# Optimization experiments

Hardware: AMD Instinct MI355X
Metric: run time of the kernel (lower is better)

## Reference

```python
import jax, jax.numpy as jnp
import numpy as np

N_NODES = 50000
N_EDGES = 800000
C_IN = 64
C_OUT = 64
K = 3


def setup_inputs() -> dict:
    key = jax.random.key(0)
    k1, k2, k3, k4, k5, k6 = jax.random.split(key, 6)
    x = jax.random.normal(k1, (N_NODES, C_IN), dtype=jnp.float32)
    edge_index = jax.random.randint(k2, (2, N_EDGES), 0, N_NODES, dtype=jnp.int32)
    edge_weight = jax.random.uniform(k3, (N_EDGES,), dtype=jnp.float32)
    # Xavier-uniform init for [K, C_IN, C_OUT] (fan over last two dims)
    limit = float(np.sqrt(6.0 / (C_IN + C_OUT)))
    theta_forward = jax.random.uniform(k4, (K, C_IN, C_OUT), minval=-limit, maxval=limit, dtype=jnp.float32)
    theta_backward = jax.random.uniform(k5, (K, C_IN, C_OUT), minval=-limit, maxval=limit, dtype=jnp.float32)
    return {
        "x": x,
        "edge_index": edge_index,
        "edge_weight": edge_weight,
        "theta_forward": theta_forward,
        "theta_backward": theta_backward,
    }


def _propagate(x, row, col, edge_weight, n_nodes):
    # degree normalization: deg[i] = sum of edge_weight over edges with row == i
    deg = jax.ops.segment_sum(edge_weight, row, num_segments=n_nodes)
    deg_inv = jnp.where(deg > 0, jax.lax.rsqrt(jnp.where(deg > 0, deg, 1.0)), 0.0)
    norm = deg_inv[row] * edge_weight * deg_inv[col]      # [E]
    msg = norm[:, None] * x[col]                          # [E, C] gather-scale
    return jax.ops.segment_sum(msg, row, num_segments=n_nodes)  # scatter-add -> [N, C]


def reference(x, edge_index, edge_weight, theta_forward, theta_backward):
    row, col = edge_index[0], edge_index[1]
    n_nodes = x.shape[0]
    k = theta_forward.shape[0]
    Tx_0 = x
    Tx_1 = _propagate(x, row, col, edge_weight, n_nodes)
    out = Tx_0 @ theta_forward[0] + Tx_1 @ theta_backward[0]
    for i in range(1, k):
        Tx_2 = _propagate(Tx_1, row, col, edge_weight, n_nodes)
        out = out + Tx_2 @ theta_forward[i] + Tx_1 @ theta_backward[i]
        Tx_1 = Tx_2
    return out
```

## Files before the change

### kernel.cpp

```cpp
#include <hip/hip_runtime.h>
#include <hip/hip_fp16.h>


#define N_NODES 50000
#define N_EDGES 800000
#define C 64
#define CAP 64
#define NPART 196
#define CAPP 4608
#define EPB 8192
#define NEB 98
#define XH_BLOCKS 782
#define CW_BLOCKS 16
#define NPADL 50176
#define NSLICE 4
#define PB 3125
#define GB 782

typedef _Float16 half8 __attribute__((ext_vector_type(8)));
typedef float f32x4 __attribute__((ext_vector_type(4)));

__global__ __launch_bounds__(1024) void scatter2_kernel(
        const int* __restrict__ row, const int* __restrict__ col,
        const float* __restrict__ w, int* __restrict__ percur,
        uint2* __restrict__ pedges,
        const float* __restrict__ x, __half* __restrict__ xh,
        const float* __restrict__ tf, const float* __restrict__ tb,
        _Float16* __restrict__ whc) {
    const int tid = threadIdx.x;
    if (blockIdx.x >= NEB + XH_BLOCKS) {
        int idx = (blockIdx.x - NEB - XH_BLOCKS) * 1024 + tid;
        int j = idx >> 12;
        int rem = idx & 4095;
        int ci = rem >> 6;
        int co = rem & 63;
        float v;
        if (j == 0)      v = tf[rem];
        else if (j == 1) v = tb[rem] + tb[4096 + rem];
        else if (j == 2) v = tf[4096 + rem] + tb[8192 + rem];
        else             v = tf[8192 + rem];
        whc[(j << 12) + (co << 6) + ci] = (_Float16)v;
        return;
    }
    if (blockIdx.x >= NEB) {
        int i = (blockIdx.x - NEB) * 1024 + tid;
        if (i < N_NODES * C / 4) {
            float4 v = ((const float4*)x)[i];
            union { float2 f2; __half2 h2[2]; } u;
            u.h2[0] = __floats2half2_rn(v.x, v.y);
            u.h2[1] = __floats2half2_rn(v.z, v.w);
            int node = i >> 4;
            int ci0 = (i & 15) << 2;
            int slice = ci0 >> 4;
            int off = ci0 & 15;
            *(float2*)(void*)(xh + (((size_t)slice * NPADL + node) << 4) + off)
                = u.f2;
        }
        return;
    }
    __shared__ int h[NPART];
    __shared__ int cur[NPART];
    uint2 ent[8];
    int pp[8];
    if (tid < NPART) h[tid] = 0;
    __syncthreads();
    int base = blockIdx.x * EPB;
#pragma unroll
    for (int i = 0; i < 8; ++i) {
        int e = base + i * 1024 + tid;
        pp[i] = -1;
        if (e < N_EDGES) {
            int r = row[e];
            unsigned int c = (unsigned int)col[e];
            unsigned int wh = (unsigned int)__half_as_ushort(__float2half_rn(w[e]));
            ent[i] = make_uint2((c << 16) | wh, (unsigned int)(r & 255));
            pp[i] = r >> 8;
            atomicAdd(&h[pp[i]], 1);
        }
    }
    __syncthreads();
    if (tid < NPART) cur[tid] = atomicAdd(&percur[tid], h[tid]);
    __syncthreads();
#pragma unroll
    for (int i = 0; i < 8; ++i) {
        if (pp[i] >= 0) {
            int slot = atomicAdd(&cur[pp[i]], 1);
            pedges[(size_t)pp[i] * CAPP + slot] = ent[i];
        }
    }
}

__global__ __launch_bounds__(1024) void build_kernel(
        const uint2* __restrict__ pedges, const int* __restrict__ percur,
        unsigned int* __restrict__ bkt, int* __restrict__ cnt,
        float* __restrict__ dinv) {
    __shared__ unsigned int lbuck[256 * CAP];
    __shared__ int lcnt[256];
    const int tid = threadIdx.x;
    const int p = blockIdx.x;
    if (tid < 256) lcnt[tid] = 0;
    __syncthreads();
    int e = min(percur[p], CAPP);
    const uint2* src = pedges + (size_t)p * CAPP;
    for (int i = tid; i < e; i += 1024) {
        uint2 en = src[i];
        int rl = (int)en.y;
        int slot = atomicAdd(&lcnt[rl], 1);
        if (slot < CAP) lbuck[(rl << 6) + slot] = en.x;
    }
    __syncthreads();
    if (tid < 256) {
        int m = min(lcnt[tid], CAP);
        int g = (p << 8) + tid;
        float sum = 0.f;
        for (int j = 0; j < m; ++j)
            sum += __half2float(__ushort_as_half(
                (unsigned short)(lbuck[(tid << 6) + j] & 0xFFFFu)));
        if (g < N_NODES) {
            cnt[g] = m;
            dinv[g] = (sum > 0.f) ? rsqrtf(sum) : 0.f;
        }
    }
    __syncthreads();
    {
        int r = tid >> 2;
        int ch = tid & 3;
        int m = min(lcnt[r], CAP);
        const uint4* s4 = (const uint4*)&lbuck[r << 6];
        uint4* dst = (uint4*)(bkt + (((size_t)(p << 8) + r) << 6));
        for (int j = ch; (j << 2) < m; j += 4) dst[j] = s4[j];
    }
}

__global__ __launch_bounds__(1024) void decode_kernel(
        const unsigned int* __restrict__ bkt, const int* __restrict__ cnt,
        const float* __restrict__ dinv, unsigned int* __restrict__ bkt2) {
    int e = blockIdx.x * 1024 + threadIdx.x;
    int node = e >> 6;
    int j = e & 63;
    if (node < N_NODES && j < min(cnt[node], CAP)) {
        unsigned int b = bkt[e];
        int c = (int)(b >> 16);
        float nn = __half2float(__ushort_as_half((unsigned short)(b & 0xFFFFu)))
                   * dinv[c];
        bkt2[e] = ((unsigned int)c << 16) |
                  (unsigned int)__half_as_ushort(__float2half_rn(nn));
    }
}

__global__ __launch_bounds__(256) void prop_kernel(
        const __half* __restrict__ xin, __half* __restrict__ xout,
        const int* __restrict__ cnt, const unsigned int* __restrict__ bkt2,
        const float* __restrict__ dinv) {
    const int tid = threadIdx.x;
    const int wib = tid >> 6;
    const int lane = tid & 63;
    const int q = lane >> 4;
    const int ql = lane & 15;
    const int u = ql >> 2;
    const int cq = ql & 3;
    const int slice = blockIdx.x & 3;
    const int tile = blockIdx.x >> 2;
    const int node = (tile << 4) + (wib << 2) + q;
    const int m = min(cnt[node], CAP);
    const int base = node << 6;
    int cj[4];
    float nj[4];
#pragma unroll
    for (int s = 0; s < 4; ++s) {
        int idx = (s << 4) + ql;
        cj[s] = 0;
        nj[s] = 0.f;
        if (idx < m) {
            unsigned int b = bkt2[base + idx];
            cj[s] = (int)(b >> 16) << 4;
            nj[s] = __half2float(__ushort_as_half((unsigned short)(b & 0xFFFFu)));
        }
    }
    int mx = m;
    mx = max(mx, __shfl_xor(mx, 16));
    mx = max(mx, __shfl_xor(mx, 32));
    const __half* xsl = xin + ((size_t)slice * NPADL << 4);
    float a0 = 0.f, a1 = 0.f, a2 = 0.f, a3 = 0.f;
    {
        int cs[8];
        float ns[8];
        float2 vs[8];
#pragma unroll
        for (int g = 0; g < 2; ++g)
#pragma unroll
            for (int t = 0; t < 4; ++t) {
                int i = (g << 2) + t;
                int sl = (q << 4) + (t << 2) + u;
                cs[i] = __shfl(cj[g], sl);
                ns[i] = __shfl(nj[g], sl);
            }
#pragma unroll
        for (int i = 0; i < 8; ++i)
            vs[i] = *(const float2*)(xsl + cs[i] + (cq << 2));
#pragma unroll
        for (int i = 0; i < 8; ++i) {
            const __half2* hp = (const __half2*)&vs[i];
            float2 A = __half22float2(hp[0]);
            float2 B = __half22float2(hp[1]);
            a0 += ns[i] * A.x;
            a1 += ns[i] * A.y;
            a2 += ns[i] * B.x;
            a3 += ns[i] * B.y;
        }
    }
    if (mx > 32) {
        int cs[8];
        float ns[8];
        float2 vs[8];
#pragma unroll
        for (int g = 0; g < 2; ++g)
#pragma unroll
            for (int t = 0; t < 4; ++t) {
                int i = (g << 2) + t;
                int sl = (q << 4) + (t << 2) + u;
                cs[i] = __shfl(cj[2 + g], sl);
                ns[i] = __shfl(nj[2 + g], sl);
            }
#pragma unroll
        for (int i = 0; i < 8; ++i)
            vs[i] = *(const float2*)(xsl + cs[i] + (cq << 2));
#pragma unroll
        for (int i = 0; i < 8; ++i) {
            const __half2* hp = (const __half2*)&vs[i];
            float2 A = __half22float2(hp[0]);
            float2 B = __half22float2(hp[1]);
            a0 += ns[i] * A.x;
            a1 += ns[i] * A.y;
            a2 += ns[i] * B.x;
            a3 += ns[i] * B.y;
        }
    }
    a0 += __shfl_xor(a0, 4); a0 += __shfl_xor(a0, 8);
    a1 += __shfl_xor(a1, 4); a1 += __shfl_xor(a1, 8);
    a2 += __shfl_xor(a2, 4); a2 += __shfl_xor(a2, 8);
    a3 += __shfl_xor(a3, 4); a3 += __shfl_xor(a3, 8);
    if (u == 0) {
        float dr = dinv[node];
        union { float2 f2; __half2 h2[2]; } o;
        o.h2[0] = __floats2half2_rn(dr * a0, dr * a1);
        o.h2[1] = __floats2half2_rn(dr * a2, dr * a3);
        *(float2*)(void*)(xout + (((size_t)slice * NPADL + node) << 4)
                          + (cq << 2)) = o.f2;
    }
}

__global__ __launch_bounds__(256) void gemm_mfma_kernel(
        const __half* __restrict__ x0, const __half* __restrict__ x1,
        const __half* __restrict__ x2, const __half* __restrict__ x3,
        const _Float16* __restrict__ whc, float* __restrict__ out) {
    const int tid = threadIdx.x;
    const int wv = tid >> 6;
    const int lane = tid & 63;
    const int quad = lane >> 4;
    const int l16 = lane & 15;
    const int mbase = (blockIdx.x << 6) + (wv << 4);
    const __half* srcs[4] = {x0, x1, x2, x3};
    f32x4 acc0 = {}, acc1 = {}, acc2 = {}, acc3 = {};
    const int arow = mbase + l16;
    const bool aok = arow < N_NODES;
    const half8 zero8 = {};
#pragma unroll
    for (int j = 0; j < 4; ++j) {
        const __half* src = srcs[j];
#pragma unroll
        for (int kk = 0; kk < 64; kk += 32) {
            const int k0 = kk + (quad << 3);
            const int slice = k0 >> 4;
            const int koff = k0 & 15;
            half8 af = aok ? *(const half8*)(const void*)(
                src + (((size_t)slice * NPADL + arow) << 4) + koff) : zero8;
            const _Float16* wb = whc + (j << 12) + kk + (quad << 3);
            half8 b0 = *(const half8*)(const void*)(wb + ((0 * 16 + l16) << 6));
            half8 b1 = *(const half8*)(const void*)(wb + ((1 * 16 + l16) << 6));
            half8 b2 = *(const half8*)(const void*)(wb + ((2 * 16 + l16) << 6));
            half8 b3 = *(const half8*)(const void*)(wb + ((3 * 16 + l16) << 6));
            acc0 = __builtin_amdgcn_mfma_f32_16x16x32_f16(af, b0, acc0, 0, 0, 0);
            acc1 = __builtin_amdgcn_mfma_f32_16x16x32_f16(af, b1, acc1, 0, 0, 0);
            acc2 = __builtin_amdgcn_mfma_f32_16x16x32_f16(af, b2, acc2, 0, 0, 0);
            acc3 = __builtin_amdgcn_mfma_f32_16x16x32_f16(af, b3, acc3, 0, 0, 0);
        }
    }
#pragma unroll
    for (int i = 0; i < 4; ++i) {
        int r = mbase + (quad << 2) + i;
        if (r < N_NODES) {
            float* dst = out + ((size_t)r << 6) + l16;
            dst[0]  = acc0[i];
            dst[16] = acc1[i];
            dst[32] = acc2[i];
            dst[48] = acc3[i];
        }
    }
}

extern "C" void kernel_launch(void* const* d_in, const int* in_sizes, int n_in,
                              void* d_out, int out_size, void* d_ws, size_t ws_size,
                              hipStream_t stream) {
    const float* x  = (const float*)d_in[0];
    const int*   ei = (const int*)d_in[1];
    const float* ew = (const float*)d_in[2];
    const float* tf = (const float*)d_in[3];
    const float* tb = (const float*)d_in[4];
    float* out = (float*)d_out;

    const int* row = ei;
    const int* col = ei + N_EDGES;

    const size_t TBL = (size_t)NSLICE * NPADL * 16 / 2;
    float* ws = (float*)d_ws;
    size_t off = 0;
    int*    percur = (int*)(ws + off); off += 256;
    uint2*  pedges = (uint2*)(ws + off); off += (size_t)NPART * CAPP * 2;
    unsigned int* bkt  = (unsigned int*)(ws + off); off += (size_t)NPADL * CAP;
    unsigned int* bkt2 = (unsigned int*)(ws + off); off += (size_t)NPADL * CAP;
    int*    cnt  = (int*)(ws + off); off += NPADL;
    float*  dinv = ws + off; off += NPADL;
    __half* xh   = (__half*)(ws + off); off += TBL;
    __half* tA   = (__half*)(ws + off); off += TBL;
    __half* tB   = (__half*)(ws + off); off += TBL;
    __half* tC   = (__half*)(ws + off); off += TBL;
    _Float16* whc = (_Float16*)(ws + off); off += 4 * 64 * 64 / 2;

    hipMemsetAsync(percur, 0, 256 * sizeof(int), stream);

    scatter2_kernel<<<NEB + XH_BLOCKS + CW_BLOCKS, 1024, 0, stream>>>(
        row, col, ew, percur, pedges, x, xh, tf, tb, whc);
    build_kernel<<<NPART, 1024, 0, stream>>>(pedges, percur, bkt, cnt, dinv);
    decode_kernel<<<NPADL * CAP / 1024, 1024, 0, stream>>>(bkt, cnt, dinv, bkt2);

    prop_kernel<<<NSLICE * PB, 256, 0, stream>>>(xh, tA, cnt, bkt2, dinv);
    prop_kernel<<<NSLICE * PB, 256, 0, stream>>>(tA, tB, cnt, bkt2, dinv);
    prop_kernel<<<NSLICE * PB, 256, 0, stream>>>(tB, tC, cnt, bkt2, dinv);

    gemm_mfma_kernel<<<GB, 256, 0, stream>>>(xh, tA, tB, tC, whc, out);
}
```

Measured before the change: 185.4 us.

## Compact per-node edge buckets into CSR layout via two-level prefix scan

Replaces the fixed 64-slot-per-node bucket layout read by the propagation kernels with a compact CSR layout. Offsets come from a per-partition block scan in build_kernel plus a new single-block scan over partition totals. Each node's edges become contiguous with its neighbours' edges, so the three prop passes read fewer, denser cache lines of edge data. The cost is an extra tiny kernel launch, extra scan barriers in build, and two more index loads per node in prop.

```diff
diff --git a/kernel.cpp b/kernel.cpp
--- a/kernel.cpp
+++ b/kernel.cpp
@@ -93,9 +93,11 @@
 __global__ __launch_bounds__(1024) void build_kernel(
         const uint2* __restrict__ pedges, const int* __restrict__ percur,
         unsigned int* __restrict__ bkt, int* __restrict__ cnt,
-        float* __restrict__ dinv) {
+        float* __restrict__ dinv, int* __restrict__ loc,
+        int* __restrict__ tot) {
     __shared__ unsigned int lbuck[256 * CAP];
     __shared__ int lcnt[256];
+    __shared__ int sscan[256];
     const int tid = threadIdx.x;
     const int p = blockIdx.x;
     if (tid < 256) lcnt[tid] = 0;
@@ -120,6 +122,21 @@
             cnt[g] = m;
             dinv[g] = (sum > 0.f) ? rsqrtf(sum) : 0.f;
         }
+        sscan[tid] = m;
+    }
+    __syncthreads();
+#pragma unroll
+    for (int d = 1; d < 256; d <<= 1) {
+        int t = 0;
+        if (tid < 256 && tid >= d) t = sscan[tid - d];
+        __syncthreads();
+        if (tid < 256) sscan[tid] += t;
+        __syncthreads();
+    }
+    if (tid < 256) {
+        int m = min(lcnt[tid], CAP);
+        loc[(p << 8) + tid] = sscan[tid] - m;
+        if (tid == 255) tot[p] = sscan[255];
     }
     __syncthreads();
     {
@@ -132,9 +149,27 @@
     }
 }
 
+__global__ __launch_bounds__(256) void scan2_kernel(
+        const int* __restrict__ tot, int* __restrict__ btot) {
+    __shared__ int s[256];
+    const int tid = threadIdx.x;
+    int v = (tid < NPART) ? tot[tid] : 0;
+    s[tid] = v;
+    __syncthreads();
+#pragma unroll
+    for (int d = 1; d < 256; d <<= 1) {
+        int t = (tid >= d) ? s[tid - d] : 0;
+        __syncthreads();
+        s[tid] += t;
+        __syncthreads();
+    }
+    if (tid < NPART) btot[tid] = s[tid] - v;
+}
+
 __global__ __launch_bounds__(1024) void decode_kernel(
         const unsigned int* __restrict__ bkt, const int* __restrict__ cnt,
-        const float* __restrict__ dinv, unsigned int* __restrict__ bkt2) {
+        const float* __restrict__ dinv, const int* __restrict__ loc,
+        const int* __restrict__ btot, unsigned int* __restrict__ bkt2) {
     int e = blockIdx.x * 1024 + threadIdx.x;
     int node = e >> 6;
     int j = e & 63;
@@ -143,7 +178,7 @@
         int c = (int)(b >> 16);
         float nn = __half2float(__ushort_as_half((unsigned short)(b & 0xFFFFu)))
                    * dinv[c];
-        bkt2[e] = ((unsigned int)c << 16) |
+        bkt2[btot[node >> 8] + loc[node] + j] = ((unsigned int)c << 16) |
                   (unsigned int)__half_as_ushort(__float2half_rn(nn));
     }
 }
@@ -151,7 +186,8 @@
 __global__ __launch_bounds__(256) void prop_kernel(
         const __half* __restrict__ xin, __half* __restrict__ xout,
         const int* __restrict__ cnt, const unsigned int* __restrict__ bkt2,
-        const float* __restrict__ dinv) {
+        const float* __restrict__ dinv, const int* __restrict__ loc,
+        const int* __restrict__ btot) {
     const int tid = threadIdx.x;
     const int wib = tid >> 6;
     const int lane = tid & 63;
@@ -163,7 +199,7 @@
     const int tile = blockIdx.x >> 2;
     const int node = (tile << 4) + (wib << 2) + q;
     const int m = min(cnt[node], CAP);
-    const int base = node << 6;
+    const int csr = btot[node >> 8] + loc[node];
     int cj[4];
     float nj[4];
 #pragma unroll
@@ -172,7 +208,7 @@
         cj[s] = 0;
         nj[s] = 0.f;
         if (idx < m) {
-            unsigned int b = bkt2[base + idx];
+            unsigned int b = bkt2[csr + idx];
             cj[s] = (int)(b >> 16) << 4;
             nj[s] = __half2float(__ushort_as_half((unsigned short)(b & 0xFFFFu)));
         }
@@ -316,10 +352,13 @@
     float* ws = (float*)d_ws;
     size_t off = 0;
     int*    percur = (int*)(ws + off); off += 256;
+    int*    tot    = (int*)(ws + off); off += 256;
+    int*    btot   = (int*)(ws + off); off += 256;
     uint2*  pedges = (uint2*)(ws + off); off += (size_t)NPART * CAPP * 2;
     unsigned int* bkt  = (unsigned int*)(ws + off); off += (size_t)NPADL * CAP;
     unsigned int* bkt2 = (unsigned int*)(ws + off); off += (size_t)NPADL * CAP;
     int*    cnt  = (int*)(ws + off); off += NPADL;
+    int*    loc  = (int*)(ws + off); off += NPADL;
     float*  dinv = ws + off; off += NPADL;
     __half* xh   = (__half*)(ws + off); off += TBL;
     __half* tA   = (__half*)(ws + off); off += TBL;
@@ -331,12 +370,18 @@
 
     scatter2_kernel<<<NEB + XH_BLOCKS + CW_BLOCKS, 1024, 0, stream>>>(
         row, col, ew, percur, pedges, x, xh, tf, tb, whc);
-    build_kernel<<<NPART, 1024, 0, stream>>>(pedges, percur, bkt, cnt, dinv);
-    decode_kernel<<<NPADL * CAP / 1024, 1024, 0, stream>>>(bkt, cnt, dinv, bkt2);
-
-    prop_kernel<<<NSLICE * PB, 256, 0, stream>>>(xh, tA, cnt, bkt2, dinv);
-    prop_kernel<<<NSLICE * PB, 256, 0, stream>>>(tA, tB, cnt, bkt2, dinv);
-    prop_kernel<<<NSLICE * PB, 256, 0, stream>>>(tB, tC, cnt, bkt2, dinv);
+    build_kernel<<<NPART, 1024, 0, stream>>>(pedges, percur, bkt, cnt, dinv,
+                                             loc, tot);
+    scan2_kernel<<<1, 256, 0, stream>>>(tot, btot);
+    decode_kernel<<<NPADL * CAP / 1024, 1024, 0, stream>>>(
+        bkt, cnt, dinv, loc, btot, bkt2);
+
+    prop_kernel<<<NSLICE * PB, 256, 0, stream>>>(
+        xh, tA, cnt, bkt2, dinv, loc, btot);
+    prop_kernel<<<NSLICE * PB, 256, 0, stream>>>(
+        tA, tB, cnt, bkt2, dinv, loc, btot);
+    prop_kernel<<<NSLICE * PB, 256, 0, stream>>>(
+        tB, tC, cnt, bkt2, dinv, loc, btot);
 
     gemm_mfma_kernel<<<GB, 256, 0, stream>>>(xh, tA, tB, tC, whc, out);
 }
```

Measured after the change: 190.4 us. +2.7%, slower.
